# Performance work log

Hardware: AMD Instinct MI355X
Metric: run time of the kernel (lower is better)

## Reference

```python
import jax, jax.numpy as jnp
import numpy as np

B, E, WIN, DX, DZ, RAW = 2048, 32, 10, 14, 14, 22

def _leaky(x):
    return jnp.where(x >= 0, x, 0.01 * x)

def setup_inputs():
    key = jax.random.key(0)
    ks = jax.random.split(key, 20)
    def w(k, i, o):
        return jax.random.normal(k, (i, o), dtype=jnp.float32) / np.float32(np.sqrt(i))
    def b(k, o):
        return jax.random.normal(k, (o,), dtype=jnp.float32) * 0.01
    return {
        "raw_obs": jax.random.normal(ks[0], (B, WIN, 1, RAW), dtype=jnp.float32),
        "state_prev": jax.random.normal(ks[1], (B, E, WIN, DX), dtype=jnp.float32),
        "pm_w1": w(ks[2], WIN * DX, 256), "pm_b1": b(ks[3], 256),
        "pm_w3": w(ks[4], 256, 512), "pm_b3": b(ks[5], 512),
        "pm_wm2": w(ks[6], 512, DX), "pm_bm2": b(ks[7], DX),
        "sm_w2": w(ks[8], WIN * RAW, 256), "sm_b2": b(ks[9], 256),
        "sm_w3": w(ks[10], 256, 256), "sm_b3": b(ks[11], 256),
        "sm_w5": w(ks[12], 256, 64), "sm_b5": b(ks[13], 64),
        "sm_w6": w(ks[14], 64, DZ), "sm_b6": b(ks[15], DZ),
        "on_w1": w(ks[16], DZ, 32), "on_b1": b(ks[17], 32),
        "on_w2": w(ks[18], 32, DZ), "on_b2": b(ks[19], DZ),
    }

def reference(raw_obs, state_prev, pm_w1, pm_b1, pm_w3, pm_b3, pm_wm2, pm_bm2,
              sm_w2, sm_b2, sm_w3, sm_b3, sm_w5, sm_b5, sm_w6, sm_b6,
              on_w1, on_b1, on_w2, on_b2):
    bs, ens, win, dx = state_prev.shape
    dz = sm_w6.shape[1]
    # --- process model (LinearFlipout evaluated at mean weights) ---
    x = state_prev.reshape(bs * ens, win * dx)
    x = _leaky(x @ pm_w1 + pm_b1)
    x = _leaky(x @ pm_w3 + pm_b3)
    state_pred = (x @ pm_wm2 + pm_bm2).reshape(bs, ens, dx)   # [B,E,dx]
    state_m = state_pred.mean(axis=1)                          # [B,dx]
    A = state_pred - state_m[:, None, :]                       # [B,E,dx]
    # --- sensor model: torch repeat(E,1,1,1) tiles ensemble-major, the final
    # reshape reinterprets as batch-major; replicate that layout faithfully ---
    s = jnp.tile(raw_obs, (ens, 1, 1, 1)).reshape(bs * ens, win * raw_obs.shape[-1])
    s = _leaky(s @ sm_w2 + sm_b2)
    s = _leaky(s @ sm_w3 + sm_b3)
    s = _leaky(s @ sm_w5 + sm_b5)
    s = s @ sm_w6 + sm_b6
    ensemble_z = s.reshape(bs, ens, dz)                        # [B,E,dz]
    z = ensemble_z.mean(axis=1, keepdims=True)                 # [B,1,dz]
    # --- observation noise R = diag_embed(square(mlp(z)+c) + init) ---
    r = jax.nn.relu(z @ on_w1 + on_b1) @ on_w2 + on_b2
    r = jnp.square(r + 0.001) + 0.038729833
    R = r.reshape(bs, dz)[:, :, None] * jnp.eye(dz, dtype=r.dtype)  # [B,dz,dz]
    # --- EnKF correction ---
    S = jnp.einsum('bei,bej->bij', A, A)                       # AT @ A, [B,dx,dx]
    innovation = S / (ens - 1) + R
    K = (S / (ens - 1)) @ jnp.linalg.inv(innovation)           # [B,dx,dz]
    diff = ensemble_z - state_pred                             # (y - H_XT)^T, [B,E,dz]
    gain = jnp.einsum('bij,bej->bei', K, diff)                 # [B,E,dx]
    state_corrected = state_pred + gain
    return (state_corrected,
            state_corrected.mean(axis=1, keepdims=True),
            state_m[:, None, :],
            z,
            ensemble_z)
```

## Files before the change

kernel.cpp:

```cpp
#include <hip/hip_runtime.h>

typedef unsigned short u16;
typedef __attribute__((ext_vector_type(8))) short short8;
typedef __attribute__((ext_vector_type(4))) float floatx4;

#define MFMA_BF16 __builtin_amdgcn_mfma_f32_16x16x32_bf16

__device__ __forceinline__ u16 f2bf(float f) {
    union { float f; unsigned int i; } v; v.f = f;
    unsigned int u = v.i;
    u += 0x7fffu + ((u >> 16) & 1u);
    return (u16)(u >> 16);
}
__device__ __forceinline__ float leaky(float x) { return x >= 0.f ? x : 0.01f * x; }

#define H1S 264
#define RS 232
#define XS 168
#define H3S 72

#define O1 917504
#define O2 946176
#define O3 974848
#define O4 1003520

#define PW1   0
#define PW3   40960
#define PWM2  172032
#define PSW2  180224
#define PSW3  237568
#define PSW5  303104
#define PSW6  319488
#define PTOTAL 320512
#define WS_NEEDED 641024
#define WS_BIG (641024 + 3670016)

struct PackSeg { const float* W; int K, N, S, base, count; };
struct PackArgs { PackSeg seg[7]; };

__global__ __launch_bounds__(256) void pack_all(PackArgs pa, u16* __restrict__ P) {
    int u = blockIdx.x * 256 + threadIdx.x;
    if (u >= PTOTAL) return;
#pragma unroll
    for (int i = 0; i < 7; i++) {
        if (u >= pa.seg[i].base && u < pa.seg[i].base + pa.seg[i].count) {
            int v = u - pa.seg[i].base;
            int j = v & 7;
            int l = (v >> 3) & 63;
            int ts = v >> 9;
            int s = ts % pa.seg[i].S;
            int t = ts / pa.seg[i].S;
            int k = s * 32 + (l >> 4) * 8 + j;
            int n = t * 16 + (l & 15);
            P[u] = (k < pa.seg[i].K && n < pa.seg[i].N)
                       ? f2bf(pa.seg[i].W[k * pa.seg[i].N + n]) : (u16)0;
            return;
        }
    }
}

__global__ __launch_bounds__(512, 4) void merged_mlp(
    const float* __restrict__ Rg, const float* __restrict__ Xg,
    const u16* __restrict__ Pk,
    const float* __restrict__ b1, const float* __restrict__ b3,
    const float* __restrict__ bm2,
    const float* __restrict__ b2, const float* __restrict__ sb3,
    const float* __restrict__ b5, const float* __restrict__ b6,
    float* __restrict__ ez_out,
    float* __restrict__ sp_ws)
{
    __shared__ __align__(16) u16 ldsH[64 * H1S];
    __shared__ __align__(16) u16 ldsC[64 * H1S];

    const int tid  = threadIdx.x;
    const int lane = tid & 63;
    const int wave = tid >> 6;
    const int q    = lane >> 4;
    const int n16  = lane & 15;

    if (blockIdx.x < 32) {
        const u16* w2p = Pk + PSW2;
        const u16* w3p = Pk + PSW3;
        const u16* w5p = Pk + PSW5;
        const u16* w6p = Pk + PSW6;
        const int row0 = blockIdx.x * 64;

        for (int idx = tid; idx < 64 * 56; idx += 512) {
            int r = idx / 56, c4 = idx - r * 56;
            float4 v = {0.f, 0.f, 0.f, 0.f};
            if (c4 < 55) v = *(const float4*)&Rg[(row0 + r) * 220 + c4 * 4];
            u16* dst = &ldsH[r * RS + c4 * 4];
            dst[0] = f2bf(v.x); dst[1] = f2bf(v.y); dst[2] = f2bf(v.z); dst[3] = f2bf(v.w);
        }
        __syncthreads();

        floatx4 acc1[4][2];
        {
            floatx4 zero = {0.f, 0.f, 0.f, 0.f};
#pragma unroll
            for (int rt = 0; rt < 4; rt++)
#pragma unroll
                for (int ct = 0; ct < 2; ct++) acc1[rt][ct] = zero;
#pragma unroll
            for (int s = 0; s < 7; s++) {
                short8 a[4];
#pragma unroll
                for (int rt = 0; rt < 4; rt++)
                    a[rt] = *(const short8*)&ldsH[(rt * 16 + n16) * RS + s * 32 + q * 8];
#pragma unroll
                for (int ct = 0; ct < 2; ct++) {
                    int t = wave * 2 + ct;
                    short8 bf = *(const short8*)&w2p[((t * 7 + s) * 64 + lane) * 8];
#pragma unroll
                    for (int rt = 0; rt < 4; rt++)
                        acc1[rt][ct] = MFMA_BF16(a[rt], bf, acc1[rt][ct], 0, 0, 0);
                }
            }
        }
        __syncthreads();
#pragma unroll
        for (int ct = 0; ct < 2; ct++) {
            int col = (wave * 2 + ct) * 16 + n16;
            float bias = b2[col];
#pragma unroll
            for (int rt = 0; rt < 4; rt++)
#pragma unroll
                for (int r = 0; r < 4; r++)
                    ldsH[(rt * 16 + q * 4 + r) * H1S + col] = f2bf(leaky(acc1[rt][ct][r] + bias));
        }
        __syncthreads();

        {
            floatx4 zero = {0.f, 0.f, 0.f, 0.f};
            floatx4 acc[4][2];
#pragma unroll
            for (int rt = 0; rt < 4; rt++)
#pragma unroll
                for (int ct = 0; ct < 2; ct++) acc[rt][ct] = zero;
#pragma unroll
            for (int s = 0; s < 8; s++) {
                short8 a[4];
#pragma unroll
                for (int rt = 0; rt < 4; rt++)
                    a[rt] = *(const short8*)&ldsH[(rt * 16 + n16) * H1S + s * 32 + q * 8];
#pragma unroll
                for (int ct = 0; ct < 2; ct++) {
                    int t = wave * 2 + ct;
                    short8 bf = *(const short8*)&w3p[((t * 8 + s) * 64 + lane) * 8];
#pragma unroll
                    for (int rt = 0; rt < 4; rt++)
                        acc[rt][ct] = MFMA_BF16(a[rt], bf, acc[rt][ct], 0, 0, 0);
                }
            }
#pragma unroll
            for (int ct = 0; ct < 2; ct++) {
                int cl = (wave * 2 + ct) * 16 + n16;
                float bias = sb3[cl];
#pragma unroll
                for (int rt = 0; rt < 4; rt++)
#pragma unroll
                    for (int r = 0; r < 4; r++)
                        ldsC[(rt * 16 + q * 4 + r) * H1S + cl] = f2bf(leaky(acc[rt][ct][r] + bias));
            }
        }
        __syncthreads();

        floatx4 acc5[4];
        {
            floatx4 zero = {0.f, 0.f, 0.f, 0.f};
#pragma unroll
            for (int rt = 0; rt < 4; rt++) acc5[rt] = zero;
            int t5 = wave >> 1, sh = wave & 1;
#pragma unroll
            for (int u = 0; u < 4; u++) {
                int s = sh * 4 + u;
                short8 bf = *(const short8*)&w5p[((t5 * 8 + s) * 64 + lane) * 8];
#pragma unroll
                for (int rt = 0; rt < 4; rt++) {
                    short8 a = *(const short8*)&ldsC[(rt * 16 + n16) * H1S + s * 32 + q * 8];
                    acc5[rt] = MFMA_BF16(a, bf, acc5[rt], 0, 0, 0);
                }
            }
        }
        {
            float* pacc = (float*)ldsH;
            int p = wave & 1, t5 = wave >> 1;
#pragma unroll
            for (int rt = 0; rt < 4; rt++)
#pragma unroll
                for (int r = 0; r < 4; r++)
                    pacc[(p * 64 + rt * 16 + q * 4 + r) * 64 + t5 * 16 + n16] = acc5[rt][r];
        }
        __syncthreads();

        {
            const float* pacc = (const float*)ldsH;
            for (int idx = tid; idx < 4096; idx += 512) {
                int row = idx >> 6, col = idx & 63;
                float v = pacc[row * 64 + col] + pacc[(64 + row) * 64 + col];
                ldsC[row * H3S + col] = f2bf(leaky(v + b5[col]));
            }
        }
        __syncthreads();

        if (wave < 4) {
            floatx4 zero = {0.f, 0.f, 0.f, 0.f};
            floatx4 acc[2] = {zero, zero};
            int s = wave & 1, rh = wave >> 1;
            short8 bf = *(const short8*)&w6p[(s * 64 + lane) * 8];
#pragma unroll
            for (int rt = 0; rt < 2; rt++) {
                short8 a = *(const short8*)&ldsC[(rh * 32 + rt * 16 + n16) * H3S + s * 32 + q * 8];
                acc[rt] = MFMA_BF16(a, bf, acc[rt], 0, 0, 0);
            }
            float* pacc2 = (float*)ldsH;
#pragma unroll
            for (int rt = 0; rt < 2; rt++)
#pragma unroll
                for (int r = 0; r < 4; r++)
                    pacc2[(s * 64 + rh * 32 + rt * 16 + q * 4 + r) * 16 + n16] = acc[rt][r];
        }
        __syncthreads();
        {
            const float* pacc2 = (const float*)ldsH;
            for (int idx = tid; idx < 1024; idx += 512) {
                int r = idx >> 4, c = idx & 15;
                float v = pacc2[r * 16 + c] + pacc2[(64 + r) * 16 + c];
                if (c < 14) ez_out[(row0 + r) * 14 + c] = v + b6[c];
            }
        }
    } else {
        const u16* w1p  = Pk + PW1;
        const u16* w3p  = Pk + PW3;
        const u16* wm2p = Pk + PWM2;
        const int bb   = blockIdx.x - 32;
        const int row0 = bb * 64;

        for (int idx = tid; idx < 64 * 42; idx += 512) {
            int r = idx / 42, c4 = idx - r * 42;
            float4 v = {0.f, 0.f, 0.f, 0.f};
            if (c4 < 35) v = *(const float4*)&Xg[(row0 + r) * 140 + c4 * 4];
            u16* dst = &ldsH[r * XS + c4 * 4];
            dst[0] = f2bf(v.x); dst[1] = f2bf(v.y); dst[2] = f2bf(v.z); dst[3] = f2bf(v.w);
        }
        __syncthreads();

        floatx4 acc1[4][2];
        {
            floatx4 zero = {0.f, 0.f, 0.f, 0.f};
#pragma unroll
            for (int rt = 0; rt < 4; rt++)
#pragma unroll
                for (int ct = 0; ct < 2; ct++) acc1[rt][ct] = zero;
#pragma unroll
            for (int s = 0; s < 5; s++) {
                short8 a[4];
#pragma unroll
                for (int rt = 0; rt < 4; rt++)
                    a[rt] = *(const short8*)&ldsH[(rt * 16 + n16) * XS + s * 32 + q * 8];
#pragma unroll
                for (int ct = 0; ct < 2; ct++) {
                    int t = wave * 2 + ct;
                    short8 bf = *(const short8*)&w1p[((t * 5 + s) * 64 + lane) * 8];
#pragma unroll
                    for (int rt = 0; rt < 4; rt++)
                        acc1[rt][ct] = MFMA_BF16(a[rt], bf, acc1[rt][ct], 0, 0, 0);
                }
            }
        }
        __syncthreads();
#pragma unroll
        for (int ct = 0; ct < 2; ct++) {
            int col = (wave * 2 + ct) * 16 + n16;
            float bias = b1[col];
#pragma unroll
            for (int rt = 0; rt < 4; rt++)
#pragma unroll
                for (int r = 0; r < 4; r++)
                    ldsH[(rt * 16 + q * 4 + r) * H1S + col] = f2bf(leaky(acc1[rt][ct][r] + bias));
        }
        __syncthreads();

        floatx4 acc3[2];
        {
            floatx4 zero = {0.f, 0.f, 0.f, 0.f};
            acc3[0] = zero; acc3[1] = zero;
        }
        const int h = wave >> 2;
        const int pg = wave & 3;
#pragma unroll
        for (int c = 0; c < 2; c++) {
            floatx4 zero = {0.f, 0.f, 0.f, 0.f};
            floatx4 acc[4][2];
#pragma unroll
            for (int rt = 0; rt < 4; rt++)
#pragma unroll
                for (int ct = 0; ct < 2; ct++) acc[rt][ct] = zero;
#pragma unroll
            for (int s = 0; s < 8; s++) {
                short8 a[4];
#pragma unroll
                for (int rt = 0; rt < 4; rt++)
                    a[rt] = *(const short8*)&ldsH[(rt * 16 + n16) * H1S + s * 32 + q * 8];
#pragma unroll
                for (int ct = 0; ct < 2; ct++) {
                    int tg = c * 16 + wave * 2 + ct;
                    short8 bf = *(const short8*)&w3p[((tg * 8 + s) * 64 + lane) * 8];
#pragma unroll
                    for (int rt = 0; rt < 4; rt++)
                        acc[rt][ct] = MFMA_BF16(a[rt], bf, acc[rt][ct], 0, 0, 0);
                }
            }
#pragma unroll
            for (int ct = 0; ct < 2; ct++) {
                int cl = (wave * 2 + ct) * 16 + n16;
                float bias = b3[c * 256 + cl];
#pragma unroll
                for (int rt = 0; rt < 4; rt++)
#pragma unroll
                    for (int r = 0; r < 4; r++)
                        ldsC[(rt * 16 + q * 4 + r) * H1S + cl] = f2bf(leaky(acc[rt][ct][r] + bias));
            }
            __syncthreads();
#pragma unroll
            for (int u = 0; u < 2; u++) {
                int sgl = pg * 2 + u;
                short8 bf = *(const short8*)&wm2p[((c * 8 + sgl) * 64 + lane) * 8];
#pragma unroll
                for (int rt = 0; rt < 2; rt++) {
                    short8 a = *(const short8*)&ldsC[(h * 32 + rt * 16 + n16) * H1S + sgl * 32 + q * 8];
                    acc3[rt] = MFMA_BF16(a, bf, acc3[rt], 0, 0, 0);
                }
            }
            __syncthreads();
        }

        {
            float* pacc = (float*)ldsH;
#pragma unroll
            for (int rt = 0; rt < 2; rt++)
#pragma unroll
                for (int r = 0; r < 4; r++)
                    pacc[(pg * 64 + h * 32 + rt * 16 + q * 4 + r) * 16 + n16] = acc3[rt][r];
        }
        __syncthreads();
        {
            const float* pacc = (const float*)ldsH;
            for (int idx = tid; idx < 1024; idx += 512) {
                int r = idx >> 4, c = idx & 15;
                float v = pacc[r * 16 + c] + pacc[(64 + r) * 16 + c]
                        + pacc[(128 + r) * 16 + c] + pacc[(192 + r) * 16 + c];
                if (c < 14) sp_ws[(row0 + r) * 14 + c] = v + bm2[c];
            }
        }
    }
}

__global__ __launch_bounds__(256) void enkf_tail(
    const float* __restrict__ sp_all,
    const float* __restrict__ on_w1, const float* __restrict__ on_b1,
    const float* __restrict__ on_w2, const float* __restrict__ on_b2,
    float* out)
{
    __shared__ float spv[32][14];
    __shared__ float ezv[32][14];
    __shared__ float smv[14], zzv[14], rrv[14];
    __shared__ float M[14][14];
    __shared__ float G[14][28];
    __shared__ float Kmat[14][14];
    __shared__ float fac[14];
    __shared__ float hbuf[32];

    const int tid = threadIdx.x;
    const int b = blockIdx.x;

    for (int idx = tid; idx < 448; idx += 256) ((float*)spv)[idx] = sp_all[b * 448 + idx];
    {
        const float* ezsrc = out + O4 + (b & 63) * 448;
        for (int idx = tid; idx < 448; idx += 256) ((float*)ezv)[idx] = ezsrc[idx];
    }
    __syncthreads();

    if (tid < 14) {
        float s = 0.f;
        for (int e = 0; e < 32; e++) s += spv[e][tid];
        smv[tid] = s * (1.f / 32.f);
    } else if (tid >= 32 && tid < 46) {
        int c = tid - 32;
        float s = 0.f;
        for (int e = 0; e < 32; e++) s += ezv[e][c];
        zzv[c] = s * (1.f / 32.f);
    }
    __syncthreads();

    if (tid < 196) {
        int i = tid / 14, j = tid - i * 14;
        float mi = smv[i], mj = smv[j];
        float s = 0.f;
        for (int e = 0; e < 32; e++) s += (spv[e][i] - mi) * (spv[e][j] - mj);
        M[i][j] = s * (1.f / 31.f);
    } else if (tid >= 224) {
        int l = tid - 224;
        float t = on_b1[l];
        for (int k = 0; k < 14; k++) t += zzv[k] * on_w1[k * 32 + l];
        hbuf[l] = t > 0.f ? t : 0.f;
    }
    __syncthreads();

    if (tid < 14) {
        float t = on_b2[tid];
        for (int k = 0; k < 32; k++) t += hbuf[k] * on_w2[k * 14 + tid];
        t += 0.001f;
        rrv[tid] = t * t + 0.038729833f;
    }
    __syncthreads();

    for (int idx = tid; idx < 392; idx += 256) {
        int i = idx / 28, j = idx - i * 28;
        G[i][j] = (j < 14) ? (M[i][j] + (i == j ? rrv[i] : 0.f))
                           : ((j - 14 == i) ? 1.f : 0.f);
    }
    __syncthreads();

    for (int c = 0; c < 14; c++) {
        if (tid < 64) {
            float pinv = 1.f / G[c][c];
            if (tid < 28) G[c][tid] *= pinv;
            if (tid < 14 && tid != c) fac[tid] = G[tid][c];
        }
        __syncthreads();
        for (int idx = tid; idx < 392; idx += 256) {
            int i = idx / 28, j = idx - i * 28;
            if (i != c) G[i][j] -= fac[i] * G[c][j];
        }
        __syncthreads();
    }

    if (tid < 196) {
        int i = tid / 14, j = tid - i * 14;
        float s = 0.f;
        for (int k = 0; k < 14; k++) s += M[i][k] * G[k][14 + j];
        Kmat[i][j] = s;
    }
    __syncthreads();

    for (int idx = tid; idx < 448; idx += 256) {
        int e = idx / 14, i = idx - e * 14;
        float g = 0.f;
        for (int j = 0; j < 14; j++) g += Kmat[i][j] * (ezv[e][j] - spv[e][j]);
        out[b * 448 + idx] = spv[e][i] + g;
        out[O4 + b * 448 + idx] = ezv[e][i];
    }
    if (tid < 14) {
        float g = 0.f;
        for (int j = 0; j < 14; j++) g += Kmat[tid][j] * (zzv[j] - smv[j]);
        out[O1 + b * 14 + tid] = smv[tid] + g;
        out[O2 + b * 14 + tid] = smv[tid];
        out[O3 + b * 14 + tid] = zzv[tid];
    }
}

extern "C" void kernel_launch(void* const* d_in, const int* in_sizes, int n_in,
                              void* d_out, int out_size, void* d_ws, size_t ws_size,
                              hipStream_t stream) {
    (void)in_sizes; (void)n_in; (void)out_size; (void)ws_size;

    const float* raw_obs    = (const float*)d_in[0];
    const float* state_prev = (const float*)d_in[1];
    const float* pm_w1  = (const float*)d_in[2];
    const float* pm_b1  = (const float*)d_in[3];
    const float* pm_w3  = (const float*)d_in[4];
    const float* pm_b3  = (const float*)d_in[5];
    const float* pm_wm2 = (const float*)d_in[6];
    const float* pm_bm2 = (const float*)d_in[7];
    const float* sm_w2  = (const float*)d_in[8];
    const float* sm_b2  = (const float*)d_in[9];
    const float* sm_w3  = (const float*)d_in[10];
    const float* sm_b3  = (const float*)d_in[11];
    const float* sm_w5  = (const float*)d_in[12];
    const float* sm_b5  = (const float*)d_in[13];
    const float* sm_w6  = (const float*)d_in[14];
    const float* sm_b6  = (const float*)d_in[15];
    const float* on_w1  = (const float*)d_in[16];
    const float* on_b1  = (const float*)d_in[17];
    const float* on_w2  = (const float*)d_in[18];
    const float* on_b2  = (const float*)d_in[19];

    float* out = (float*)d_out;
    u16* P = (u16*)d_ws;
    float* sp_ws = (float*)((char*)d_ws + WS_NEEDED);

    PackArgs pa;
    pa.seg[0] = { pm_w1,  140, 256, 5,  PW1,  40960  };
    pa.seg[1] = { pm_w3,  256, 512, 8,  PW3,  131072 };
    pa.seg[2] = { pm_wm2, 512, 14,  16, PWM2, 8192   };
    pa.seg[3] = { sm_w2,  220, 256, 7,  PSW2, 57344  };
    pa.seg[4] = { sm_w3,  256, 256, 8,  PSW3, 65536  };
    pa.seg[5] = { sm_w5,  256, 64,  8,  PSW5, 16384  };
    pa.seg[6] = { sm_w6,  64,  14,  2,  PSW6, 1024   };
    pack_all<<<(PTOTAL + 255) / 256, 256, 0, stream>>>(pa, P);

    merged_mlp<<<1056, 512, 0, stream>>>(raw_obs, state_prev, P,
                                         pm_b1, pm_b3, pm_bm2,
                                         sm_b2, sm_b3, sm_b5, sm_b6,
                                         out + O4, sp_ws);
    enkf_tail<<<2048, 256, 0, stream>>>(sp_ws, on_w1, on_b1, on_w2, on_b2, out);
}
```

Before: 166.8 us.

## Chunk hidden layers to halve LDS buffer and raise occupancy

Halves the second LDS buffer (stride 136 instead of 264) by computing the 256/512-wide hidden layers in 128-column chunks. Each chunk is consumed right away by the next layer's MFMAs, which accumulate in registers. Waves now split 2 row-halves by 4 column groups instead of owning all 64 rows. Together with the smaller accumulator arrays, this lets launch bounds request 6 blocks per SM instead of 4, aiming for more occupancy and fewer LDS partial-sum passes. The cost is extra __syncthreads per chunk and more redundant A-fragment loads per wave.

```diff
diff --git a/kernel.cpp b/kernel.cpp
--- a/kernel.cpp
+++ b/kernel.cpp
@@ -18,6 +18,7 @@
 #define RS 232
 #define XS 168
 #define H3S 72
+#define CS 136
 
 #define O1 917504
 #define O2 946176
@@ -59,7 +60,7 @@
     }
 }
 
-__global__ __launch_bounds__(512, 4) void merged_mlp(
+__global__ __launch_bounds__(512, 6) void merged_mlp(
     const float* __restrict__ Rg, const float* __restrict__ Xg,
     const u16* __restrict__ Pk,
     const float* __restrict__ b1, const float* __restrict__ b3,
@@ -70,13 +71,15 @@
     float* __restrict__ sp_ws)
 {
     __shared__ __align__(16) u16 ldsH[64 * H1S];
-    __shared__ __align__(16) u16 ldsC[64 * H1S];
+    __shared__ __align__(16) u16 ldsC[64 * CS];
 
     const int tid  = threadIdx.x;
     const int lane = tid & 63;
     const int wave = tid >> 6;
     const int q    = lane >> 4;
     const int n16  = lane & 15;
+    const int rh   = wave >> 2;
+    const int cg   = wave & 3;
 
     if (blockIdx.x < 32) {
         const u16* w2p = Pk + PSW2;
@@ -130,102 +133,87 @@
         }
         __syncthreads();
 
-        {
-            floatx4 zero = {0.f, 0.f, 0.f, 0.f};
-            floatx4 acc[4][2];
-#pragma unroll
-            for (int rt = 0; rt < 4; rt++)
+        floatx4 acc5[2];
+        {
+            floatx4 zero = {0.f, 0.f, 0.f, 0.f};
+            acc5[0] = zero; acc5[1] = zero;
+        }
+#pragma unroll
+        for (int c = 0; c < 2; c++) {
+            floatx4 zero = {0.f, 0.f, 0.f, 0.f};
+            floatx4 acc[2][2];
+#pragma unroll
+            for (int rt = 0; rt < 2; rt++)
 #pragma unroll
                 for (int ct = 0; ct < 2; ct++) acc[rt][ct] = zero;
 #pragma unroll
             for (int s = 0; s < 8; s++) {
-                short8 a[4];
-#pragma unroll
-                for (int rt = 0; rt < 4; rt++)
-                    a[rt] = *(const short8*)&ldsH[(rt * 16 + n16) * H1S + s * 32 + q * 8];
+                short8 a[2];
+#pragma unroll
+                for (int rt = 0; rt < 2; rt++)
+                    a[rt] = *(const short8*)&ldsH[(rh * 32 + rt * 16 + n16) * H1S + s * 32 + q * 8];
 #pragma unroll
                 for (int ct = 0; ct < 2; ct++) {
-                    int t = wave * 2 + ct;
-                    short8 bf = *(const short8*)&w3p[((t * 8 + s) * 64 + lane) * 8];
-#pragma unroll
-                    for (int rt = 0; rt < 4; rt++)
+                    int tg = c * 8 + cg * 2 + ct;
+                    short8 bf = *(const short8*)&w3p[((tg * 8 + s) * 64 + lane) * 8];
+#pragma unroll
+                    for (int rt = 0; rt < 2; rt++)
                         acc[rt][ct] = MFMA_BF16(a[rt], bf, acc[rt][ct], 0, 0, 0);
                 }
             }
 #pragma unroll
             for (int ct = 0; ct < 2; ct++) {
-                int cl = (wave * 2 + ct) * 16 + n16;
-                float bias = sb3[cl];
-#pragma unroll
-                for (int rt = 0; rt < 4; rt++)
+                int cl = (cg * 2 + ct) * 16 + n16;
+                float bias = sb3[c * 128 + cl];
+#pragma unroll
+                for (int rt = 0; rt < 2; rt++)
 #pragma unroll
                     for (int r = 0; r < 4; r++)
-                        ldsC[(rt * 16 + q * 4 + r) * H1S + cl] = f2bf(leaky(acc[rt][ct][r] + bias));
-            }
-        }
-        __syncthreads();
-
-        floatx4 acc5[4];
-        {
-            floatx4 zero = {0.f, 0.f, 0.f, 0.f};
-#pragma unroll
-            for (int rt = 0; rt < 4; rt++) acc5[rt] = zero;
-            int t5 = wave >> 1, sh = wave & 1;
+                        ldsC[(rh * 32 + rt * 16 + q * 4 + r) * CS + cl] = f2bf(leaky(acc[rt][ct][r] + bias));
+            }
+            __syncthreads();
 #pragma unroll
             for (int u = 0; u < 4; u++) {
-                int s = sh * 4 + u;
-                short8 bf = *(const short8*)&w5p[((t5 * 8 + s) * 64 + lane) * 8];
-#pragma unroll
-                for (int rt = 0; rt < 4; rt++) {
-                    short8 a = *(const short8*)&ldsC[(rt * 16 + n16) * H1S + s * 32 + q * 8];
+                int sg = c * 4 + u;
+                short8 bf = *(const short8*)&w5p[((cg * 8 + sg) * 64 + lane) * 8];
+#pragma unroll
+                for (int rt = 0; rt < 2; rt++) {
+                    short8 a = *(const short8*)&ldsC[(rh * 32 + rt * 16 + n16) * CS + u * 32 + q * 8];
                     acc5[rt] = MFMA_BF16(a, bf, acc5[rt], 0, 0, 0);
                 }
             }
-        }
-        {
-            float* pacc = (float*)ldsH;
-            int p = wave & 1, t5 = wave >> 1;
-#pragma unroll
-            for (int rt = 0; rt < 4; rt++)
+            __syncthreads();
+        }
+
+        {
+            int col = cg * 16 + n16;
+            float bias = b5[col];
+#pragma unroll
+            for (int rt = 0; rt < 2; rt++)
 #pragma unroll
                 for (int r = 0; r < 4; r++)
-                    pacc[(p * 64 + rt * 16 + q * 4 + r) * 64 + t5 * 16 + n16] = acc5[rt][r];
-        }
-        __syncthreads();
-
-        {
-            const float* pacc = (const float*)ldsH;
-            for (int idx = tid; idx < 4096; idx += 512) {
-                int row = idx >> 6, col = idx & 63;
-                float v = pacc[row * 64 + col] + pacc[(64 + row) * 64 + col];
-                ldsC[row * H3S + col] = f2bf(leaky(v + b5[col]));
-            }
-        }
-        __syncthreads();
-
-        if (wave < 4) {
-            floatx4 zero = {0.f, 0.f, 0.f, 0.f};
-            floatx4 acc[2] = {zero, zero};
-            int s = wave & 1, rh = wave >> 1;
+                    ldsC[(rh * 32 + rt * 16 + q * 4 + r) * H3S + col] = f2bf(leaky(acc5[rt][r] + bias));
+        }
+        __syncthreads();
+
+        {
+            floatx4 zero = {0.f, 0.f, 0.f, 0.f};
+            floatx4 acc = zero;
+            int s = wave & 1, rq = wave >> 1;
             short8 bf = *(const short8*)&w6p[(s * 64 + lane) * 8];
-#pragma unroll
-            for (int rt = 0; rt < 2; rt++) {
-                short8 a = *(const short8*)&ldsC[(rh * 32 + rt * 16 + n16) * H3S + s * 32 + q * 8];
-                acc[rt] = MFMA_BF16(a, bf, acc[rt], 0, 0, 0);
-            }
+            short8 a = *(const short8*)&ldsC[(rq * 16 + n16) * H3S + s * 32 + q * 8];
+            acc = MFMA_BF16(a, bf, acc, 0, 0, 0);
             float* pacc2 = (float*)ldsH;
 #pragma unroll
-            for (int rt = 0; rt < 2; rt++)
-#pragma unroll
-                for (int r = 0; r < 4; r++)
-                    pacc2[(s * 64 + rh * 32 + rt * 16 + q * 4 + r) * 16 + n16] = acc[rt][r];
+            for (int r = 0; r < 4; r++)
+                pacc2[(s * 64 + rq * 16 + q * 4 + r) * 16 + n16] = acc[r];
         }
         __syncthreads();
         {
             const float* pacc2 = (const float*)ldsH;
             for (int idx = tid; idx < 1024; idx += 512) {
                 int r = idx >> 4, c = idx & 15;
-                float v = pacc2[r * 16 + c] + pacc2[(64 + r) * 16 + c];
+                float v = pacc2[idx] + pacc2[1024 + idx];
                 if (c < 14) ez_out[(row0 + r) * 14 + c] = v + b6[c];
             }
         }
@@ -286,49 +274,45 @@
             floatx4 zero = {0.f, 0.f, 0.f, 0.f};
             acc3[0] = zero; acc3[1] = zero;
         }
-        const int h = wave >> 2;
-        const int pg = wave & 3;
-#pragma unroll
-        for (int c = 0; c < 2; c++) {
-            floatx4 zero = {0.f, 0.f, 0.f, 0.f};
-            floatx4 acc[4][2];
-#pragma unroll
-            for (int rt = 0; rt < 4; rt++)
+#pragma unroll
+        for (int c = 0; c < 4; c++) {
+            floatx4 zero = {0.f, 0.f, 0.f, 0.f};
+            floatx4 acc[2][2];
+#pragma unroll
+            for (int rt = 0; rt < 2; rt++)
 #pragma unroll
                 for (int ct = 0; ct < 2; ct++) acc[rt][ct] = zero;
 #pragma unroll
             for (int s = 0; s < 8; s++) {
-                short8 a[4];
-#pragma unroll
-                for (int rt = 0; rt < 4; rt++)
-                    a[rt] = *(const short8*)&ldsH[(rt * 16 + n16) * H1S + s * 32 + q * 8];
+                short8 a[2];
+#pragma unroll
+                for (int rt = 0; rt < 2; rt++)
+                    a[rt] = *(const short8*)&ldsH[(rh * 32 + rt * 16 + n16) * H1S + s * 32 + q * 8];
 #pragma unroll
                 for (int ct = 0; ct < 2; ct++) {
-                    int tg = c * 16 + wave * 2 + ct;
+                    int tg = c * 8 + cg * 2 + ct;
                     short8 bf = *(const short8*)&w3p[((tg * 8 + s) * 64 + lane) * 8];
 #pragma unroll
-                    for (int rt = 0; rt < 4; rt++)
+                    for (int rt = 0; rt < 2; rt++)
                         acc[rt][ct] = MFMA_BF16(a[rt], bf, acc[rt][ct], 0, 0, 0);
                 }
             }
 #pragma unroll
             for (int ct = 0; ct < 2; ct++) {
-                int cl = (wave * 2 + ct) * 16 + n16;
-                float bias = b3[c * 256 + cl];
-#pragma unroll
-                for (int rt = 0; rt < 4; rt++)
+                int cl = (cg * 2 + ct) * 16 + n16;
+                float bias = b3[c * 128 + cl];
+#pragma unroll
+                for (int rt = 0; rt < 2; rt++)
 #pragma unroll
                     for (int r = 0; r < 4; r++)
-                        ldsC[(rt * 16 + q * 4 + r) * H1S + cl] = f2bf(leaky(acc[rt][ct][r] + bias));
+                        ldsC[(rh * 32 + rt * 16 + q * 4 + r) * CS + cl] = f2bf(leaky(acc[rt][ct][r] + bias));
             }
             __syncthreads();
-#pragma unroll
-            for (int u = 0; u < 2; u++) {
-                int sgl = pg * 2 + u;
-                short8 bf = *(const short8*)&wm2p[((c * 8 + sgl) * 64 + lane) * 8];
+            {
+                short8 bf = *(const short8*)&wm2p[((c * 4 + cg) * 64 + lane) * 8];
 #pragma unroll
                 for (int rt = 0; rt < 2; rt++) {
-                    short8 a = *(const short8*)&ldsC[(h * 32 + rt * 16 + n16) * H1S + sgl * 32 + q * 8];
+                    short8 a = *(const short8*)&ldsC[(rh * 32 + rt * 16 + n16) * CS + cg * 32 + q * 8];
                     acc3[rt] = MFMA_BF16(a, bf, acc3[rt], 0, 0, 0);
                 }
             }
@@ -341,15 +325,14 @@
             for (int rt = 0; rt < 2; rt++)
 #pragma unroll
                 for (int r = 0; r < 4; r++)
-                    pacc[(pg * 64 + h * 32 + rt * 16 + q * 4 + r) * 16 + n16] = acc3[rt][r];
+                    pacc[(cg * 64 + rh * 32 + rt * 16 + q * 4 + r) * 16 + n16] = acc3[rt][r];
         }
         __syncthreads();
         {
             const float* pacc = (const float*)ldsH;
             for (int idx = tid; idx < 1024; idx += 512) {
                 int r = idx >> 4, c = idx & 15;
-                float v = pacc[r * 16 + c] + pacc[(64 + r) * 16 + c]
-                        + pacc[(128 + r) * 16 + c] + pacc[(192 + r) * 16 + c];
+                float v = pacc[idx] + pacc[1024 + idx] + pacc[2048 + idx] + pacc[3072 + idx];
                 if (c < 14) sp_ws[(row0 + r) * 14 + c] = v + bm2[c];
             }
         }
```

Result: slower. 175.9 us (+5.5%).

## Process 128 rows per block in process-model MLP to double weight reuse

Applied to the files above, without the earlier changes.

The process-model branch of the merged MLP now handles 128 rows per block instead of 64. The eight waves are split into two row halves and four column groups, so each wave does 4x4 MFMA tiles and each weight fragment loaded from global memory is reused across twice as many rows. LDS buffers double and launch bounds drop to 2 blocks per CU, which lowers occupancy and raises register pressure. The sensor branch's final layer is also respread across all eight waves.

```diff
diff --git a/kernel.cpp b/kernel.cpp
--- a/kernel.cpp
+++ b/kernel.cpp
@@ -59,7 +59,7 @@
     }
 }
 
-__global__ __launch_bounds__(512, 4) void merged_mlp(
+__global__ __launch_bounds__(512, 2) void merged_mlp(
     const float* __restrict__ Rg, const float* __restrict__ Xg,
     const u16* __restrict__ Pk,
     const float* __restrict__ b1, const float* __restrict__ b3,
@@ -69,14 +69,16 @@
     float* __restrict__ ez_out,
     float* __restrict__ sp_ws)
 {
-    __shared__ __align__(16) u16 ldsH[64 * H1S];
-    __shared__ __align__(16) u16 ldsC[64 * H1S];
+    __shared__ __align__(16) u16 ldsH[128 * H1S];
+    __shared__ __align__(16) u16 ldsC[128 * H1S];
 
     const int tid  = threadIdx.x;
     const int lane = tid & 63;
     const int wave = tid >> 6;
     const int q    = lane >> 4;
     const int n16  = lane & 15;
+    const int rh   = wave >> 2;
+    const int cg   = wave & 3;
 
     if (blockIdx.x < 32) {
         const u16* w2p = Pk + PSW2;
@@ -203,29 +205,24 @@
         }
         __syncthreads();
 
-        if (wave < 4) {
-            floatx4 zero = {0.f, 0.f, 0.f, 0.f};
-            floatx4 acc[2] = {zero, zero};
-            int s = wave & 1, rh = wave >> 1;
+        {
+            floatx4 zero = {0.f, 0.f, 0.f, 0.f};
+            floatx4 acc = zero;
+            int s = wave & 1, rq = wave >> 1;
             short8 bf = *(const short8*)&w6p[(s * 64 + lane) * 8];
-#pragma unroll
-            for (int rt = 0; rt < 2; rt++) {
-                short8 a = *(const short8*)&ldsC[(rh * 32 + rt * 16 + n16) * H3S + s * 32 + q * 8];
-                acc[rt] = MFMA_BF16(a, bf, acc[rt], 0, 0, 0);
-            }
+            short8 a = *(const short8*)&ldsC[(rq * 16 + n16) * H3S + s * 32 + q * 8];
+            acc = MFMA_BF16(a, bf, acc, 0, 0, 0);
             float* pacc2 = (float*)ldsH;
 #pragma unroll
-            for (int rt = 0; rt < 2; rt++)
-#pragma unroll
-                for (int r = 0; r < 4; r++)
-                    pacc2[(s * 64 + rh * 32 + rt * 16 + q * 4 + r) * 16 + n16] = acc[rt][r];
+            for (int r = 0; r < 4; r++)
+                pacc2[(s * 64 + rq * 16 + q * 4 + r) * 16 + n16] = acc[r];
         }
         __syncthreads();
         {
             const float* pacc2 = (const float*)ldsH;
             for (int idx = tid; idx < 1024; idx += 512) {
                 int r = idx >> 4, c = idx & 15;
-                float v = pacc2[r * 16 + c] + pacc2[(64 + r) * 16 + c];
+                float v = pacc2[idx] + pacc2[1024 + idx];
                 if (c < 14) ez_out[(row0 + r) * 14 + c] = v + b6[c];
             }
         }
@@ -234,9 +231,9 @@
         const u16* w3p  = Pk + PW3;
         const u16* wm2p = Pk + PWM2;
         const int bb   = blockIdx.x - 32;
-        const int row0 = bb * 64;
-
-        for (int idx = tid; idx < 64 * 42; idx += 512) {
+        const int row0 = bb * 128;
+
+        for (int idx = tid; idx < 128 * 42; idx += 512) {
             int r = idx / 42, c4 = idx - r * 42;
             float4 v = {0.f, 0.f, 0.f, 0.f};
             if (c4 < 35) v = *(const float4*)&Xg[(row0 + r) * 140 + c4 * 4];
@@ -245,22 +242,22 @@
         }
         __syncthreads();
 
-        floatx4 acc1[4][2];
-        {
-            floatx4 zero = {0.f, 0.f, 0.f, 0.f};
-#pragma unroll
-            for (int rt = 0; rt < 4; rt++)
-#pragma unroll
-                for (int ct = 0; ct < 2; ct++) acc1[rt][ct] = zero;
+        floatx4 acc1[4][4];
+        {
+            floatx4 zero = {0.f, 0.f, 0.f, 0.f};
+#pragma unroll
+            for (int rt = 0; rt < 4; rt++)
+#pragma unroll
+                for (int ct = 0; ct < 4; ct++) acc1[rt][ct] = zero;
 #pragma unroll
             for (int s = 0; s < 5; s++) {
                 short8 a[4];
 #pragma unroll
                 for (int rt = 0; rt < 4; rt++)
-                    a[rt] = *(const short8*)&ldsH[(rt * 16 + n16) * XS + s * 32 + q * 8];
-#pragma unroll
-                for (int ct = 0; ct < 2; ct++) {
-                    int t = wave * 2 + ct;
+                    a[rt] = *(const short8*)&ldsH[(rh * 64 + rt * 16 + n16) * XS + s * 32 + q * 8];
+#pragma unroll
+                for (int ct = 0; ct < 4; ct++) {
+                    int t = cg * 4 + ct;
                     short8 bf = *(const short8*)&w1p[((t * 5 + s) * 64 + lane) * 8];
 #pragma unroll
                     for (int rt = 0; rt < 4; rt++)
@@ -270,41 +267,40 @@
         }
         __syncthreads();
 #pragma unroll
-        for (int ct = 0; ct < 2; ct++) {
-            int col = (wave * 2 + ct) * 16 + n16;
+        for (int ct = 0; ct < 4; ct++) {
+            int col = (cg * 4 + ct) * 16 + n16;
             float bias = b1[col];
 #pragma unroll
             for (int rt = 0; rt < 4; rt++)
 #pragma unroll
                 for (int r = 0; r < 4; r++)
-                    ldsH[(rt * 16 + q * 4 + r) * H1S + col] = f2bf(leaky(acc1[rt][ct][r] + bias));
-        }
-        __syncthreads();
-
-        floatx4 acc3[2];
-        {
-            floatx4 zero = {0.f, 0.f, 0.f, 0.f};
-            acc3[0] = zero; acc3[1] = zero;
-        }
-        const int h = wave >> 2;
-        const int pg = wave & 3;
+                    ldsH[(rh * 64 + rt * 16 + q * 4 + r) * H1S + col] = f2bf(leaky(acc1[rt][ct][r] + bias));
+        }
+        __syncthreads();
+
+        floatx4 acc3[4];
+        {
+            floatx4 zero = {0.f, 0.f, 0.f, 0.f};
+#pragma unroll
+            for (int rt = 0; rt < 4; rt++) acc3[rt] = zero;
+        }
 #pragma unroll
         for (int c = 0; c < 2; c++) {
             floatx4 zero = {0.f, 0.f, 0.f, 0.f};
-            floatx4 acc[4][2];
-#pragma unroll
-            for (int rt = 0; rt < 4; rt++)
-#pragma unroll
-                for (int ct = 0; ct < 2; ct++) acc[rt][ct] = zero;
+            floatx4 acc[4][4];
+#pragma unroll
+            for (int rt = 0; rt < 4; rt++)
+#pragma unroll
+                for (int ct = 0; ct < 4; ct++) acc[rt][ct] = zero;
 #pragma unroll
             for (int s = 0; s < 8; s++) {
                 short8 a[4];
 #pragma unroll
                 for (int rt = 0; rt < 4; rt++)
-                    a[rt] = *(const short8*)&ldsH[(rt * 16 + n16) * H1S + s * 32 + q * 8];
-#pragma unroll
-                for (int ct = 0; ct < 2; ct++) {
-                    int tg = c * 16 + wave * 2 + ct;
+                    a[rt] = *(const short8*)&ldsH[(rh * 64 + rt * 16 + n16) * H1S + s * 32 + q * 8];
+#pragma unroll
+                for (int ct = 0; ct < 4; ct++) {
+                    int tg = c * 16 + cg * 4 + ct;
                     short8 bf = *(const short8*)&w3p[((tg * 8 + s) * 64 + lane) * 8];
 #pragma unroll
                     for (int rt = 0; rt < 4; rt++)
@@ -312,23 +308,23 @@
                 }
             }
 #pragma unroll
-            for (int ct = 0; ct < 2; ct++) {
-                int cl = (wave * 2 + ct) * 16 + n16;
+            for (int ct = 0; ct < 4; ct++) {
+                int cl = (cg * 4 + ct) * 16 + n16;
                 float bias = b3[c * 256 + cl];
 #pragma unroll
                 for (int rt = 0; rt < 4; rt++)
 #pragma unroll
                     for (int r = 0; r < 4; r++)
-                        ldsC[(rt * 16 + q * 4 + r) * H1S + cl] = f2bf(leaky(acc[rt][ct][r] + bias));
+                        ldsC[(rh * 64 + rt * 16 + q * 4 + r) * H1S + cl] = f2bf(leaky(acc[rt][ct][r] + bias));
             }
             __syncthreads();
 #pragma unroll
-            for (int u = 0; u < 2; u++) {
-                int sgl = pg * 2 + u;
-                short8 bf = *(const short8*)&wm2p[((c * 8 + sgl) * 64 + lane) * 8];
-#pragma unroll
-                for (int rt = 0; rt < 2; rt++) {
-                    short8 a = *(const short8*)&ldsC[(h * 32 + rt * 16 + n16) * H1S + sgl * 32 + q * 8];
+            for (int uu = 0; uu < 2; uu++) {
+                int u = cg * 2 + uu;
+                short8 bf = *(const short8*)&wm2p[((c * 8 + u) * 64 + lane) * 8];
+#pragma unroll
+                for (int rt = 0; rt < 4; rt++) {
+                    short8 a = *(const short8*)&ldsC[(rh * 64 + rt * 16 + n16) * H1S + u * 32 + q * 8];
                     acc3[rt] = MFMA_BF16(a, bf, acc3[rt], 0, 0, 0);
                 }
             }
@@ -338,18 +334,17 @@
         {
             float* pacc = (float*)ldsH;
 #pragma unroll
-            for (int rt = 0; rt < 2; rt++)
+            for (int rt = 0; rt < 4; rt++)
 #pragma unroll
                 for (int r = 0; r < 4; r++)
-                    pacc[(pg * 64 + h * 32 + rt * 16 + q * 4 + r) * 16 + n16] = acc3[rt][r];
+                    pacc[(cg * 128 + rh * 64 + rt * 16 + q * 4 + r) * 16 + n16] = acc3[rt][r];
         }
         __syncthreads();
         {
             const float* pacc = (const float*)ldsH;
-            for (int idx = tid; idx < 1024; idx += 512) {
+            for (int idx = tid; idx < 2048; idx += 512) {
                 int r = idx >> 4, c = idx & 15;
-                float v = pacc[r * 16 + c] + pacc[(64 + r) * 16 + c]
-                        + pacc[(128 + r) * 16 + c] + pacc[(192 + r) * 16 + c];
+                float v = pacc[idx] + pacc[2048 + idx] + pacc[4096 + idx] + pacc[6144 + idx];
                 if (c < 14) sp_ws[(row0 + r) * 14 + c] = v + bm2[c];
             }
         }
@@ -500,9 +495,9 @@
     pa.seg[6] = { sm_w6,  64,  14,  2,  PSW6, 1024   };
     pack_all<<<(PTOTAL + 255) / 256, 256, 0, stream>>>(pa, P);
 
-    merged_mlp<<<1056, 512, 0, stream>>>(raw_obs, state_prev, P,
-                                         pm_b1, pm_b3, pm_bm2,
-                                         sm_b2, sm_b3, sm_b5, sm_b6,
-                                         out + O4, sp_ws);
+    merged_mlp<<<544, 512, 0, stream>>>(raw_obs, state_prev, P,
+                                        pm_b1, pm_b3, pm_bm2,
+                                        sm_b2, sm_b3, sm_b5, sm_b6,
+                                        out + O4, sp_ws);
     enkf_tail<<<2048, 256, 0, stream>>>(sp_ws, on_w1, on_b1, on_w2, on_b2, out);
 }
```

After: 179.0 us. 7.3% more time.
